# Kernel optimization log

Hardware: AMD Instinct MI355X
Metric: run time of the kernel (lower is better)

The kernel has to match this reference:

```python
import jax, jax.numpy as jnp
import numpy as np

IMG = 800          # image size (square)
STRIDE = 4         # feature-map stride
S = 14             # rcnn_crop_size
C = 256            # crop_channels
N = 512            # number of rpn proposals
NUM_CLASSES = 81   # COCO (incl. background at index 0)
HID = 1024
NMS_TH = 0.5
SCORE_TH = 0.05


def setup_inputs() -> dict:
    key = jax.random.key(0)
    ks = jax.random.split(key, 8)
    features = jax.random.normal(ks[0], (1, C, IMG // STRIDE, IMG // STRIDE), jnp.float32)
    # valid proposal boxes (x0, y0, x1, y1) in image coordinates
    u = jax.random.uniform(ks[1], (N, 4), jnp.float32)
    x0 = u[:, 0] * (IMG - 64.0)
    y0 = u[:, 1] * (IMG - 64.0)
    bw = 16.0 + u[:, 2] * 240.0
    bh = 16.0 + u[:, 3] * 240.0
    proposals = jnp.stack([x0, y0, jnp.minimum(x0 + bw, IMG - 1.0), jnp.minimum(y0 + bh, IMG - 1.0)], axis=1)
    d1 = C * S * S  # 50176
    w1 = jax.random.normal(ks[2], (d1, HID), jnp.float32) * (1.0 / np.sqrt(d1))
    b1 = jnp.zeros((HID,), jnp.float32)
    w2 = jax.random.normal(ks[3], (HID, HID), jnp.float32) * (1.0 / np.sqrt(HID))
    b2 = jnp.zeros((HID,), jnp.float32)
    w_cls = jax.random.normal(ks[4], (HID, NUM_CLASSES), jnp.float32) * (1.0 / np.sqrt(HID))
    b_cls = jnp.zeros((NUM_CLASSES,), jnp.float32)
    w_reg = jax.random.normal(ks[5], (HID, NUM_CLASSES * 4), jnp.float32) * (1.0 / np.sqrt(HID))
    b_reg = jnp.zeros((NUM_CLASSES * 4,), jnp.float32)
    return dict(features=features, proposals=proposals, w1=w1, b1=b1, w2=w2, b2=b2,
                w_cls=w_cls, b_cls=b_cls, w_reg=w_reg, b_reg=b_reg)


def roi_align(feat, boxes):
    """feat: [C,H,W]; boxes: [N,4] image coords -> crops [N,C,S,S] via bilinear sampling (1 sample per bin)."""
    _, H, W = feat.shape
    b = boxes / STRIDE
    t = (jnp.arange(S, dtype=feat.dtype) + 0.5) / S                # [S] bin centers
    xs = b[:, 0:1] + (b[:, 2:3] - b[:, 0:1]) * t                   # [N,S]
    ys = b[:, 1:2] + (b[:, 3:4] - b[:, 1:2]) * t                   # [N,S]
    xx = jnp.broadcast_to(xs[:, None, :], (boxes.shape[0], S, S))  # [N,S,S]
    yy = jnp.broadcast_to(ys[:, :, None], (boxes.shape[0], S, S))
    x0f = jnp.floor(xx); y0f = jnp.floor(yy)
    fx = xx - x0f; fy = yy - y0f
    x0i = jnp.clip(x0f.astype(jnp.int32), 0, W - 1); x1i = jnp.clip(x0i + 1, 0, W - 1)
    y0i = jnp.clip(y0f.astype(jnp.int32), 0, H - 1); y1i = jnp.clip(y0i + 1, 0, H - 1)
    # gathers -> [C,N,S,S]
    v = (((1 - fx) * (1 - fy))[None] * feat[:, y0i, x0i]
         + (fx * (1 - fy))[None] * feat[:, y0i, x1i]
         + ((1 - fx) * fy)[None] * feat[:, y1i, x0i]
         + (fx * fy)[None] * feat[:, y1i, x1i])
    return v.transpose(1, 0, 2, 3)  # [N,C,S,S]


def decode_boxes(rois, d):
    w = rois[:, 2] - rois[:, 0]; h = rois[:, 3] - rois[:, 1]
    cx = rois[:, 0] + 0.5 * w; cy = rois[:, 1] + 0.5 * h
    px = cx + d[:, 0] * w; py = cy + d[:, 1] * h
    pw = w * jnp.exp(jnp.clip(d[:, 2], -4.0, 4.0))
    ph = h * jnp.exp(jnp.clip(d[:, 3], -4.0, 4.0))
    b = jnp.stack([px - 0.5 * pw, py - 0.5 * ph, px + 0.5 * pw, py + 0.5 * ph], axis=1)
    return jnp.clip(b, 0.0, IMG - 1.0)


def iou_matrix(b):
    area = jnp.maximum(b[:, 2] - b[:, 0], 0.0) * jnp.maximum(b[:, 3] - b[:, 1], 0.0)
    ix0 = jnp.maximum(b[:, None, 0], b[None, :, 0])
    iy0 = jnp.maximum(b[:, None, 1], b[None, :, 1])
    ix1 = jnp.minimum(b[:, None, 2], b[None, :, 2])
    iy1 = jnp.minimum(b[:, None, 3], b[None, :, 3])
    inter = jnp.maximum(ix1 - ix0, 0.0) * jnp.maximum(iy1 - iy0, 0.0)
    return inter / (area[:, None] + area[None, :] - inter + 1e-6)


def reference(features, proposals, w1, b1, w2, b2, w_cls, b_cls, w_reg, b_reg):
    # 1) RoIAlign crop
    crops = roi_align(features[0], proposals)              # [N,C,S,S]
    # 2) RCNN head
    x = crops.reshape(N, -1)
    x = jax.nn.relu(x @ w1 + b1)
    x = jax.nn.relu(x @ w2 + b2)
    logits = x @ w_cls + b_cls                             # [N,81]
    deltas = (x @ w_reg + b_reg).reshape(N, NUM_CLASSES, 4)
    # 3) NMS post-processing
    probs = jax.nn.softmax(logits, axis=-1)
    fg = probs[:, 1:]                                      # exclude background
    labels = jnp.argmax(fg, axis=-1) + 1                   # [N]
    scores = jnp.max(fg, axis=-1)                          # [N]
    d = deltas[jnp.arange(N), labels]                      # per-ROI delta of predicted class
    boxes = decode_boxes(proposals, d)
    order = jnp.argsort(-scores)
    bs = boxes[order]; ss = scores[order]; ls = labels[order]
    valid = ss > SCORE_TH
    M = iou_matrix(bs)                                     # [N,N]
    idx = jnp.arange(N)
    def body(i, keep):
        alive = keep[i] & valid[i]
        supp = (M[i] > NMS_TH) & (idx > i) & alive
        return keep & (~supp)
    keep = jax.lax.fori_loop(0, N, body, valid)
    keepf = jax.lax.stop_gradient(keep.astype(bs.dtype))
    final = jnp.concatenate([bs, ss[:, None]], axis=1) * keepf[:, None]   # [N,5]
    return final, ls.astype(jnp.int32), keep
```

## Files before the change

kernel.cpp:

```cpp
#include <hip/hip_runtime.h>
#include <cstdint>

#define F_H 200
#define F_W 200
#define D1  50176
#define NBOX 512
#define NHID 1024

typedef _Float16 f16;
typedef _Float16 half8 __attribute__((ext_vector_type(8)));
typedef _Float16 half4v __attribute__((ext_vector_type(4)));
typedef _Float16 half2v __attribute__((ext_vector_type(2)));
typedef float    f32x4 __attribute__((ext_vector_type(4)));

__device__ __forceinline__ void gload16(const void* g, void* l) {
  __builtin_amdgcn_global_load_lds((const __attribute__((address_space(1))) void*)g,
                                   (__attribute__((address_space(3))) void*)l,
                                   16, 0, 0);
}

__device__ __forceinline__ half2v pkrtz(float a, float b) {
  return __builtin_bit_cast(half2v, __builtin_amdgcn_cvt_pkrtz(a, b));
}

__device__ __forceinline__ void splitf16(float v, f16& h, f16& l) {
  f16 hh = (f16)v;
  float hf = (float)hh;
  if (fabsf(hf) < 6.1035156e-5f) hf = 0.f;
  h = (f16)hh;
  if (fabsf(hf) < 6.1035156e-5f) h = (f16)0.f;
  l = (f16)((v - hf) * 2048.f);
}

__global__ __launch_bounds__(256) void k_roi(const float* __restrict__ feat,
                                             const float* __restrict__ prop,
                                             f16* __restrict__ xhi, f16* __restrict__ xlo) {
  uint32_t idx = blockIdx.x * 256u + threadIdx.x;
  uint32_t n = idx / 25088u;
  uint32_t rem = idx % 25088u;
  uint32_t c = rem / 98u;
  uint32_t r2 = rem % 98u;
  uint32_t i = r2 / 7u;
  uint32_t jp = r2 % 7u;
  float b0 = prop[n * 4 + 0] * 0.25f, b1 = prop[n * 4 + 1] * 0.25f;
  float b2 = prop[n * 4 + 2] * 0.25f, b3 = prop[n * 4 + 3] * 0.25f;
  float ty = ((float)i + 0.5f) * (1.0f / 14.0f);
  float yy = b1 + (b3 - b1) * ty;
  float y0f = floorf(yy);
  float fy = yy - y0f;
  int y0 = (int)y0f; y0 = y0 < 0 ? 0 : (y0 > F_H - 1 ? F_H - 1 : y0);
  int y1 = y0 + 1 > F_H - 1 ? F_H - 1 : y0 + 1;
  const float* fr0 = feat + (size_t)c * (F_H * F_W) + (size_t)y0 * F_W;
  const float* fr1 = feat + (size_t)c * (F_H * F_W) + (size_t)y1 * F_W;
  f16 hs[2], ls[2];
#pragma unroll
  for (int e = 0; e < 2; ++e) {
    uint32_t j = jp * 2u + (uint32_t)e;
    float tx = ((float)j + 0.5f) * (1.0f / 14.0f);
    float xx = b0 + (b2 - b0) * tx;
    float x0f = floorf(xx);
    float fx = xx - x0f;
    int x0 = (int)x0f; x0 = x0 < 0 ? 0 : (x0 > F_W - 1 ? F_W - 1 : x0);
    int x1 = x0 + 1 > F_W - 1 ? F_W - 1 : x0 + 1;
    float v00 = fr0[x0], v01 = fr0[x1], v10 = fr1[x0], v11 = fr1[x1];
    float v = (1.f - fx) * (1.f - fy) * v00 + fx * (1.f - fy) * v01 +
              (1.f - fx) * fy * v10 + fx * fy * v11;
    splitf16(v, hs[e], ls[e]);
  }
  uint32_t base = n * 50176u + c * 196u + i * 14u + jp * 2u;
  half2v hv; hv[0] = hs[0]; hv[1] = hs[1];
  half2v lv; lv[0] = ls[0]; lv[1] = ls[1];
  *(half2v*)(xhi + base) = hv;
  *(half2v*)(xlo + base) = lv;
}

__global__ __launch_bounds__(256) void k_tsplit(const float* __restrict__ W,
                                                f16* __restrict__ hiT, f16* __restrict__ loT,
                                                int Kdim, int Ndim) {
  __shared__ f16 lh[64 * 72];
  __shared__ f16 ll[64 * 72];
  int t = threadIdx.x;
  int k0 = blockIdx.x * 64, n0 = blockIdx.y * 64;
  int r = t >> 2, cq = t & 3;
  const float* src = W + (size_t)(k0 + r) * Ndim + n0 + cq * 16;
  f16 hv[16], lv[16];
#pragma unroll
  for (int e = 0; e < 4; ++e) {
    f32x4 v = *(const f32x4*)(src + e * 4);
#pragma unroll
    for (int x = 0; x < 4; ++x) splitf16(v[x], hv[e * 4 + x], lv[e * 4 + x]);
  }
#pragma unroll
  for (int j = 0; j < 16; ++j) {
    int n_l = cq * 16 + j;
    lh[n_l * 72 + r] = hv[j];
    ll[n_l * 72 + r] = lv[j];
  }
  __syncthreads();
  f16* oh = hiT + (size_t)(n0 + r) * Kdim + k0 + cq * 16;
  f16* ol = loT + (size_t)(n0 + r) * Kdim + k0 + cq * 16;
  *(half8*)(oh)     = *(const half8*)(&lh[r * 72 + cq * 16]);
  *(half8*)(oh + 8) = *(const half8*)(&lh[r * 72 + cq * 16 + 8]);
  *(half8*)(ol)     = *(const half8*)(&ll[r * 72 + cq * 16]);
  *(half8*)(ol + 8) = *(const half8*)(&ll[r * 72 + cq * 16 + 8]);
}

__global__ __launch_bounds__(256) void k_packT(const float* __restrict__ wc_, const float* __restrict__ bc,
                                               const float* __restrict__ wr_, const float* __restrict__ br,
                                               f16* __restrict__ whT_hi, f16* __restrict__ whT_lo,
                                               float* __restrict__ bh) {
  uint32_t idx = blockIdx.x * 256u + threadIdx.x;
  if (idx < 512u * 1024u) {
    uint32_t n = idx >> 10, k = idx & 1023u;
    float v = 0.f;
    if (n < 81u) v = wc_[k * 81u + n];
    else if (n < 405u) v = wr_[k * 324u + (n - 81u)];
    f16 h, l; splitf16(v, h, l);
    whT_hi[idx] = h; whT_lo[idx] = l;
  } else if (idx < 512u * 1024u + 512u) {
    uint32_t n = idx - 512u * 1024u;
    float v = 0.f;
    if (n < 81u) v = bc[n];
    else if (n < 405u) v = br[n - 81u];
    bh[n] = v;
  }
}

__global__ __launch_bounds__(256) void k_pack(const float* __restrict__ wc, const float* __restrict__ bc,
                                              const float* __restrict__ wr, const float* __restrict__ br,
                                              float* __restrict__ wh, float* __restrict__ bh) {
  uint32_t idx = blockIdx.x * 256u + threadIdx.x;
  if (idx < (uint32_t)NHID * 512u) {
    uint32_t k = idx >> 9, n = idx & 511u;
    float v = 0.f;
    if (n < 81u) v = wc[k * 81u + n];
    else if (n < 405u) v = wr[k * 324u + (n - 81u)];
    wh[idx] = v;
  } else if (idx < (uint32_t)NHID * 512u + 512u) {
    uint32_t n = idx - (uint32_t)NHID * 512u;
    float v = 0.f;
    if (n < 81u) v = bc[n];
    else if (n < 405u) v = br[n - 81u];
    bh[n] = v;
  }
}

__global__ __launch_bounds__(512, 2) void k_gemm2(
    const f16* __restrict__ Ahi, const f16* __restrict__ Alo,
    const f16* __restrict__ Bhi, const f16* __restrict__ Blo,
    float* __restrict__ Cp, int K, int N, int Kc, int nMt, int nNt)
{
  __shared__ char sm[131072];
  const int t = threadIdx.x;
  const int lane = t & 63;
  const int wid = t >> 6;
  const int wr = wid >> 2;
  const int wc = wid & 3;
  const int rl = lane & 15;
  const int lq = lane >> 4;

  int bid = blockIdx.x;
  int low = bid & 7, qq = bid >> 3;
  int nt = qq % nNt;
  int chi = qq / nNt;
  int c = chi * 8 + low;
  int ks = c / nMt;
  int mt = c % nMt;
  const int brow = mt * 256;
  const int nbase = nt * 256;
  const int k0 = ks * Kc;
  const int nk = Kc >> 5;

  uint32_t aoffg[2], aldso[2];
#pragma unroll
  for (int i = 0; i < 2; ++i) {
    uint32_t idx = (uint32_t)t + 512u * i;
    uint32_t q2 = idx >> 2, s = idx & 3;
    uint32_t qh = q2 >> 6;
    uint32_t grh = (qh == 1u) ? 2u : (qh == 2u) ? 1u : qh;
    uint32_t gr = grh * 64u + (q2 & 63u);
    aoffg[i] = (uint32_t)(brow + gr) * (uint32_t)K + (s ^ ((q2 >> 1) & 3u)) * 8u;
    aldso[i] = idx * 16u;
  }
  uint32_t boffg[2], bldso[2];
#pragma unroll
  for (int i = 0; i < 2; ++i) {
    uint32_t idx = (uint32_t)t + 512u * i;
    uint32_t rB = idx >> 2, s = idx & 3;
    boffg[i] = (uint32_t)(nbase + rB) * (uint32_t)K + (s ^ ((rB >> 1) & 3u)) * 8u;
    bldso[i] = idx * 16u;
  }

  const uint32_t swzk = (uint32_t)(lq ^ ((rl >> 1) & 3)) * 16u;
  const uint32_t a_off_lane = (uint32_t)(rl * 64) + swzk;
  const uint32_t b_off_lane = (uint32_t)((wc * 16 + rl) * 64) + swzk;

  f32x4 zero4 = {0.f, 0.f, 0.f, 0.f};
  f32x4 acc[8][4];
#pragma unroll
  for (int m = 0; m < 8; ++m)
#pragma unroll
    for (int n = 0; n < 4; ++n) acc[m][n] = zero4;

#define PH0STAGE(LB, KB) do { \
    gload16(Bhi + boffg[0] + (KB), (LB) + 32768 + bldso[0]); \
    gload16(Blo + boffg[0] + (KB), (LB) + 49152 + bldso[0]); \
    gload16(Bhi + boffg[1] + (KB), (LB) + 32768 + bldso[1]); \
    gload16(Blo + boffg[1] + (KB), (LB) + 49152 + bldso[1]); \
    gload16(Ahi + aoffg[0] + (KB), (LB) + aldso[0]); \
    gload16(Alo + aoffg[0] + (KB), (LB) + 16384 + aldso[0]); \
  } while (0)

#define PH1STAGE(LB, KB) do { \
    gload16(Ahi + aoffg[1] + (KB), (LB) + aldso[1]); \
    gload16(Alo + aoffg[1] + (KB), (LB) + 16384 + aldso[1]); \
  } while (0)

#define COMPUTE_PHASE(P) do { \
    half8 bh2[4], bl2[4]; \
    _Pragma("unroll") \
    for (int nf = 0; nf < 4; ++nf) { \
      bh2[nf] = *(const half8*)(lb + 32768 + nf * 4096 + b_off_lane); \
      bl2[nf] = *(const half8*)(lb + 49152 + nf * 4096 + b_off_lane); \
    } \
    __builtin_amdgcn_s_setprio(1); \
    _Pragma("unroll") \
    for (int mm = 0; mm < 4; ++mm) { \
      const char* ab = lb + (P) * 8192 + wr * 4096 + mm * 1024 + a_off_lane; \
      half8 ah = *(const half8*)(ab); \
      half8 al = *(const half8*)(ab + 16384); \
      _Pragma("unroll") \
      for (int nf = 0; nf < 4; ++nf) { \
        acc[(P)*4+mm][nf] = __builtin_amdgcn_mfma_f32_16x16x32_f16(ah, bh2[nf], acc[(P)*4+mm][nf], 0, 0, 0); \
        f32x4 tt = __builtin_amdgcn_mfma_f32_16x16x32_f16(ah, bl2[nf], zero4, 0, 0, 0); \
        tt = __builtin_amdgcn_mfma_f32_16x16x32_f16(al, bh2[nf], tt, 0, 0, 0); \
        acc[(P)*4+mm][nf] += tt * 4.8828125e-4f; \
      } \
    } \
    __builtin_amdgcn_s_setprio(0); \
  } while (0)

  PH0STAGE(sm, (uint32_t)k0);
  PH1STAGE(sm, (uint32_t)k0);

  int cur = 0;
  for (int kt = 0; kt < nk; ++kt) {
    int ktn = (kt + 1 < nk) ? kt + 1 : kt;
    uint32_t kbn = (uint32_t)(k0 + ktn * 32);
    const char* lb = sm + cur * 65536;
    char* lbn = sm + (cur ^ 1) * 65536;

    asm volatile("s_waitcnt vmcnt(2)" ::: "memory");
    __builtin_amdgcn_s_barrier();
    __builtin_amdgcn_sched_barrier(0);
    PH0STAGE(lbn, kbn);
    COMPUTE_PHASE(0);

    asm volatile("s_waitcnt vmcnt(6)" ::: "memory");
    __builtin_amdgcn_s_barrier();
    __builtin_amdgcn_sched_barrier(0);
    PH1STAGE(lbn, kbn);
    COMPUTE_PHASE(1);

    cur ^= 1;
  }

  float* Cs = Cp + (size_t)ks * ((size_t)512 * (uint32_t)N);
#pragma unroll
  for (int m = 0; m < 8; ++m) {
    int rg = brow + wr * 128 + m * 16 + lq * 4;
#pragma unroll
    for (int nf = 0; nf < 4; ++nf) {
      int cg = nbase + nf * 64 + wc * 16 + rl;
#pragma unroll
      for (int rr = 0; rr < 4; ++rr)
        Cs[(size_t)(rg + rr) * (uint32_t)N + cg] = acc[m][nf][rr];
    }
  }
#undef PH0STAGE
#undef PH1STAGE
#undef COMPUTE_PHASE
}

__global__ __launch_bounds__(512, 2) void k_gemm(
    const f16* __restrict__ Ahi, const f16* __restrict__ Alo,
    const float* __restrict__ B, float* __restrict__ Cp,
    int K, int N, int Kc, int nMt, int nNt)
{
  __shared__ char sm[131072];
  const int t = threadIdx.x;
  const int lane = t & 63;
  const int wid = t >> 6;
  const int wr = wid >> 2;
  const int wc = wid & 3;
  const int rl = lane & 15;
  const int lq = lane >> 4;

  int bid = blockIdx.x;
  int low = bid & 7, q = bid >> 3;
  int nt = q % nNt;
  int chi = q / nNt;
  int c = chi * 8 + low;
  int ks = c / nMt;
  int mt = c % nMt;
  const int brow = mt * 256;
  const int nbase = nt * 256;
  const int k0 = ks * Kc;
  const int nk = Kc >> 5;

  uint32_t aoffg[2], aldso[2];
#pragma unroll
  for (int i = 0; i < 2; ++i) {
    uint32_t idx = (uint32_t)t + 512u * i;
    uint32_t r = idx >> 2, s = idx & 3;
    uint32_t sz = s ^ ((r >> 1) & 3);
    aoffg[i] = (uint32_t)(brow + r) * (uint32_t)K + sz * 8u;
    aldso[i] = idx * 16u;
  }
  uint32_t boffg[2][2], bldso[2][2];
#pragma unroll
  for (int h = 0; h < 2; ++h)
#pragma unroll
    for (int i = 0; i < 2; ++i) {
      uint32_t idx = (uint32_t)t + 512u * i;
      uint32_t kr = idx >> 5, sg = idx & 31;
      uint32_t sgs = sg ^ (((kr >> 3) & 3) << 2);
      boffg[h][i] = kr * (uint32_t)N + (uint32_t)(nbase + h * 128) + sgs * 4u;
      bldso[h][i] = 32768u + (uint32_t)h * 16384u + idx * 16u;
    }

  const uint32_t a_off = (uint32_t)(wr * 8192 + rl * 64) + (uint32_t)((lq ^ ((rl >> 1) & 3)) * 16);
  const uint32_t b_lane = (uint32_t)((((wc ^ lq) & 3) * 16 + rl) * 4);

  f32x4 zero4 = {0.f, 0.f, 0.f, 0.f};
  f32x4 acc[8][4];
#pragma unroll
  for (int m = 0; m < 8; ++m)
#pragma unroll
    for (int n = 0; n < 4; ++n) acc[m][n] = zero4;

#define STAGE_A(LB, KB) do { \
    gload16(Ahi + aoffg[0] + (KB), (LB) + aldso[0]); \
    gload16(Alo + aoffg[0] + (KB), (LB) + 16384 + aldso[0]); \
    gload16(Ahi + aoffg[1] + (KB), (LB) + aldso[1]); \
    gload16(Alo + aoffg[1] + (KB), (LB) + 16384 + aldso[1]); \
  } while (0)

#define STAGE_B(LB, KB) do { \
    gload16(B + (size_t)(KB) * (uint32_t)N + boffg[0][0], (LB) + bldso[0][0]); \
    gload16(B + (size_t)(KB) * (uint32_t)N + boffg[0][1], (LB) + bldso[0][1]); \
    gload16(B + (size_t)(KB) * (uint32_t)N + boffg[1][0], (LB) + bldso[1][0]); \
    gload16(B + (size_t)(KB) * (uint32_t)N + boffg[1][1], (LB) + bldso[1][1]); \
  } while (0)

#define COMPUTE_PHASE(P) do { \
    half8 bhv[2], blv[2]; \
    _Pragma("unroll") \
    for (int x = 0; x < 2; ++x) { \
      const int nf = 2 * (P) + x; \
      const char* bb = lb + 32768 + (nf >> 1) * 16384 + (nf & 1) * 256 + b_lane; \
      _Pragma("unroll") \
      for (int jj = 0; jj < 8; jj += 2) { \
        float v0 = *(const float*)(bb + (lq * 8 + jj) * 512); \
        float v1 = *(const float*)(bb + (lq * 8 + jj + 1) * 512); \
        half2v hp = pkrtz(v0, v1); \
        f16 e0 = (fabsf(v0) >= 6.1035156e-5f) ? hp[0] : (f16)0; \
        f16 e1 = (fabsf(v1) >= 6.1035156e-5f) ? hp[1] : (f16)0; \
        half2v lp = pkrtz((v0 - (float)e0) * 2048.f, (v1 - (float)e1) * 2048.f); \
        bhv[x][jj] = e0; bhv[x][jj + 1] = e1; \
        blv[x][jj] = lp[0]; blv[x][jj + 1] = lp[1]; \
      } \
    } \
    __builtin_amdgcn_s_setprio(1); \
    _Pragma("unroll") \
    for (int m = 0; m < 8; ++m) { \
      half8 ah = *(const half8*)(lb + a_off + m * 1024); \
      half8 al = *(const half8*)(lb + 16384 + a_off + m * 1024); \
      _Pragma("unroll") \
      for (int x = 0; x < 2; ++x) { \
        const int nf = 2 * (P) + x; \
        acc[m][nf] = __builtin_amdgcn_mfma_f32_16x16x32_f16(ah, bhv[x], acc[m][nf], 0, 0, 0); \
        f32x4 tt = __builtin_amdgcn_mfma_f32_16x16x32_f16(ah, blv[x], zero4, 0, 0, 0); \
        tt = __builtin_amdgcn_mfma_f32_16x16x32_f16(al, bhv[x], tt, 0, 0, 0); \
        acc[m][nf] += tt * 4.8828125e-4f; \
      } \
    } \
    __builtin_amdgcn_s_setprio(0); \
  } while (0)

  STAGE_A(sm, (uint32_t)k0);
  STAGE_B(sm, (uint32_t)k0);

  int cur = 0;
  for (int kt = 0; kt < nk; ++kt) {
    int ktn = (kt + 1 < nk) ? kt + 1 : kt;
    uint32_t kbn = (uint32_t)(k0 + ktn * 32);
    const char* lb = sm + cur * 65536;
    char* lbn = sm + (cur ^ 1) * 65536;

    asm volatile("s_waitcnt vmcnt(2)" ::: "memory");
    __builtin_amdgcn_s_barrier();
    __builtin_amdgcn_sched_barrier(0);
    STAGE_A(lbn, kbn);
    COMPUTE_PHASE(0);

    asm volatile("s_waitcnt vmcnt(4)" ::: "memory");
    __builtin_amdgcn_s_barrier();
    __builtin_amdgcn_sched_barrier(0);
    STAGE_B(lbn, kbn);
    COMPUTE_PHASE(1);

    cur ^= 1;
  }

  float* Cs = Cp + (size_t)ks * ((size_t)512 * (uint32_t)N);
#pragma unroll
  for (int m = 0; m < 8; ++m) {
    int rg = brow + wr * 128 + m * 16 + lq * 4;
#pragma unroll
    for (int nf = 0; nf < 4; ++nf) {
      int cg = nbase + nf * 64 + wc * 16 + rl;
#pragma unroll
      for (int rr = 0; rr < 4; ++rr)
        Cs[(size_t)(rg + rr) * (uint32_t)N + cg] = acc[m][nf][rr];
    }
  }
#undef STAGE_A
#undef STAGE_B
#undef COMPUTE_PHASE
}

__global__ __launch_bounds__(256) void k_reduce(
    const float* __restrict__ parts, const float* __restrict__ bias,
    int nS, int MN4, int Ncols, int relu,
    float* __restrict__ outf, f16* __restrict__ ohi, f16* __restrict__ olo)
{
  uint32_t idx = blockIdx.x * 256u + threadIdx.x;
  if (idx >= (uint32_t)MN4) return;
  f32x4 s = *(const f32x4*)(bias + ((idx * 4u) % (uint32_t)Ncols));
  const f32x4* p4 = (const f32x4*)parts;
  for (int i = 0; i < nS; ++i) s += p4[(size_t)i * (uint32_t)MN4 + idx];
  if (relu) {
#pragma unroll
    for (int j = 0; j < 4; ++j) s[j] = fmaxf(s[j], 0.f);
  }
  if (outf) *(f32x4*)(outf + (size_t)idx * 4) = s;
  if (ohi) {
    half4v h, l;
#pragma unroll
    for (int j = 0; j < 4; ++j) { f16 hh, ll; splitf16(s[j], hh, ll); h[j] = hh; l[j] = ll; }
    *(half4v*)(ohi + (size_t)idx * 4) = h;
    *(half4v*)(olo + (size_t)idx * 4) = l;
  }
}

__global__ __launch_bounds__(256) void k_post(
    const float* __restrict__ ld, const float* __restrict__ prop,
    float* __restrict__ boxes, float* __restrict__ scores, int* __restrict__ labels)
{
  int n = blockIdx.x * 256 + threadIdx.x;
  if (n >= NBOX) return;
  const float* L = ld + (size_t)n * 512;
  float m = L[0];
  for (int j = 1; j < 81; ++j) m = fmaxf(m, L[j]);
  float sum = 0.f;
  for (int j = 0; j < 81; ++j) sum += expf(L[j] - m);
  float best = -1.f; int bj = 1;
  for (int j = 1; j < 81; ++j) {
    float p = expf(L[j] - m) / sum;
    if (p > best) { best = p; bj = j; }
  }
  float d0 = L[81 + bj * 4 + 0];
  float d1 = L[81 + bj * 4 + 1];
  float d2 = L[81 + bj * 4 + 2];
  float d3 = L[81 + bj * 4 + 3];
  float p0 = prop[n * 4 + 0], p1 = prop[n * 4 + 1], p2 = prop[n * 4 + 2], p3 = prop[n * 4 + 3];
  float w = p2 - p0, h = p3 - p1;
  float cx = p0 + 0.5f * w, cy = p1 + 0.5f * h;
  float px = cx + d0 * w, py = cy + d1 * h;
  float pw = w * expf(fminf(fmaxf(d2, -4.f), 4.f));
  float ph = h * expf(fminf(fmaxf(d3, -4.f), 4.f));
  float bx0 = px - 0.5f * pw, by0 = py - 0.5f * ph;
  float bx1 = px + 0.5f * pw, by1 = py + 0.5f * ph;
  boxes[n * 4 + 0] = fminf(fmaxf(bx0, 0.f), 799.f);
  boxes[n * 4 + 1] = fminf(fmaxf(by0, 0.f), 799.f);
  boxes[n * 4 + 2] = fminf(fmaxf(bx1, 0.f), 799.f);
  boxes[n * 4 + 3] = fminf(fmaxf(by1, 0.f), 799.f);
  scores[n] = best;
  labels[n] = bj;
}

__global__ __launch_bounds__(512) void k_sort(
    const float* __restrict__ scores, const float* __restrict__ boxes, const int* __restrict__ labels,
    float* __restrict__ bs, float* __restrict__ ss, int* __restrict__ ls)
{
  __shared__ unsigned long long keys[512];
  int t = threadIdx.x;
  unsigned sb = __float_as_uint(scores[t]);
  keys[t] = ((unsigned long long)(0xFFFFFFFFu - sb) << 32) | (unsigned)t;
  __syncthreads();
  for (int k = 2; k <= 512; k <<= 1) {
    for (int j = k >> 1; j > 0; j >>= 1) {
      int p = t ^ j;
      if (p > t) {
        unsigned long long a = keys[t], b = keys[p];
        bool asc = ((t & k) == 0);
        if (asc ? (a > b) : (a < b)) { keys[t] = b; keys[p] = a; }
      }
      __syncthreads();
    }
  }
  unsigned o = (unsigned)(keys[t] & 0xFFFFFFFFu);
  ss[t] = scores[o];
  ls[t] = labels[o];
  bs[t * 4 + 0] = boxes[o * 4 + 0];
  bs[t * 4 + 1] = boxes[o * 4 + 1];
  bs[t * 4 + 2] = boxes[o * 4 + 2];
  bs[t * 4 + 3] = boxes[o * 4 + 3];
}

__global__ __launch_bounds__(64) void k_mask(const float* __restrict__ bs,
                                             unsigned long long* __restrict__ mask) {
  int i = blockIdx.x;
  int lane = threadIdx.x;
  float ax0 = bs[i * 4], ay0 = bs[i * 4 + 1], ax1 = bs[i * 4 + 2], ay1 = bs[i * 4 + 3];
  float aarea = fmaxf(ax1 - ax0, 0.f) * fmaxf(ay1 - ay0, 0.f);
  for (int w = 0; w < 8; ++w) {
    int j = w * 64 + lane;
    float bx0 = bs[j * 4], by0 = bs[j * 4 + 1], bx1 = bs[j * 4 + 2], by1 = bs[j * 4 + 3];
    float barea = fmaxf(bx1 - bx0, 0.f) * fmaxf(by1 - by0, 0.f);
    float ix0 = fmaxf(ax0, bx0), iy0 = fmaxf(ay0, by0);
    float ix1 = fminf(ax1, bx1), iy1 = fminf(ay1, by1);
    float inter = fmaxf(ix1 - ix0, 0.f) * fmaxf(iy1 - iy0, 0.f);
    float iou = inter / (aarea + barea - inter + 1e-6f);
    bool cond = (iou > 0.5f) && (j > i);
    unsigned long long b = __ballot(cond);
    if (lane == 0) mask[i * 8 + w] = b;
  }
}

__global__ __launch_bounds__(64) void k_nms(const unsigned long long* __restrict__ mask,
                                            const float* __restrict__ ss,
                                            const float* __restrict__ bs,
                                            const int* __restrict__ ls,
                                            float* __restrict__ out) {
  int lane = threadIdx.x;
  unsigned long long bal[8];
  for (int w = 0; w < 8; ++w) bal[w] = __ballot(ss[w * 64 + lane] > 0.05f);
  unsigned long long keep = (lane < 8) ? bal[lane] : 0ULL;
  for (int i = 0; i < 512; ++i) {
    unsigned long long kw = __shfl(keep, i >> 6);
    if ((kw >> (i & 63)) & 1ULL) {
      unsigned long long mi = (lane < 8) ? mask[i * 8 + lane] : 0ULL;
      keep &= ~mi;
    }
  }
  __shared__ unsigned long long kws[8];
  if (lane < 8) kws[lane] = keep;
  __syncthreads();
  for (int it = 0; it < 56; ++it) {
    int idx = lane + it * 64;
    float val;
    if (idx < 2560) {
      int i = idx / 5, c2 = idx % 5;
      bool kb = (kws[i >> 6] >> (i & 63)) & 1ULL;
      val = kb ? (c2 < 4 ? bs[i * 4 + c2] : ss[i]) : 0.f;
    } else if (idx < 3072) {
      int i = idx - 2560;
      val = (float)ls[i];
    } else {
      int i = idx - 3072;
      val = ((kws[i >> 6] >> (i & 63)) & 1ULL) ? 1.f : 0.f;
    }
    out[idx] = val;
  }
}

static constexpr size_t SZ_X    = (size_t)NBOX * D1 * 2;
static constexpr size_t OFF_XHI = 0;
static constexpr size_t OFF_XLO = OFF_XHI + SZ_X;
static constexpr size_t OFF_PART = OFF_XLO + SZ_X;
static constexpr size_t SZ_PART = (size_t)32 * 512 * 1024 * 4;
static constexpr size_t SZ_H    = (size_t)512 * 1024 * 2;
static constexpr size_t OFF_H1HI = OFF_PART + SZ_PART;
static constexpr size_t OFF_H1LO = OFF_H1HI + SZ_H;
static constexpr size_t OFF_H2HI = OFF_H1LO + SZ_H;
static constexpr size_t OFF_H2LO = OFF_H2HI + SZ_H;
static constexpr size_t OFF_WH   = OFF_H2LO + SZ_H;
static constexpr size_t OFF_BH   = OFF_WH + (size_t)1024 * 512 * 4;
static constexpr size_t OFF_LD   = OFF_BH + 4096;
static constexpr size_t OFF_BOX  = OFF_LD + (size_t)512 * 512 * 4;
static constexpr size_t OFF_SC   = OFF_BOX + 512 * 4 * 4;
static constexpr size_t OFF_LB   = OFF_SC + 4096;
static constexpr size_t OFF_BS   = OFF_LB + 4096;
static constexpr size_t OFF_SS   = OFF_BS + 512 * 4 * 4;
static constexpr size_t OFF_LS   = OFF_SS + 4096;
static constexpr size_t OFF_MASK = OFF_LS + 4096;
static constexpr size_t OFF_END  = OFF_MASK + (size_t)512 * 8 * 8;

static constexpr size_t SZ_W1P   = (size_t)1024 * D1 * 2;
static constexpr size_t NP_XHI   = 0;
static constexpr size_t NP_XLO   = NP_XHI + SZ_X;
static constexpr size_t NP_W1HIT = NP_XLO + SZ_X;
static constexpr size_t NP_W1LOT = NP_W1HIT + SZ_W1P;
static constexpr size_t NP_PART  = NP_W1LOT + SZ_W1P;
static constexpr size_t NP_W2HIT = NP_PART + SZ_PART;
static constexpr size_t NP_W2LOT = NP_W2HIT + (size_t)1024 * 1024 * 2;
static constexpr size_t NP_WHHIT = NP_W2LOT + (size_t)1024 * 1024 * 2;
static constexpr size_t NP_WHLOT = NP_WHHIT + (size_t)512 * 1024 * 2;
static constexpr size_t NP_BH    = NP_WHLOT + (size_t)512 * 1024 * 2;
static constexpr size_t NP_H1HI  = NP_BH + 4096;
static constexpr size_t NP_H1LO  = NP_H1HI + SZ_H;
static constexpr size_t NP_H2HI  = NP_H1LO + SZ_H;
static constexpr size_t NP_H2LO  = NP_H2HI + SZ_H;
static constexpr size_t NP_LD    = NP_H2LO + SZ_H;
static constexpr size_t NP_BOX   = NP_LD + (size_t)512 * 512 * 4;
static constexpr size_t NP_SC    = NP_BOX + 512 * 4 * 4;
static constexpr size_t NP_LB    = NP_SC + 4096;
static constexpr size_t NP_BS    = NP_LB + 4096;
static constexpr size_t NP_SS    = NP_BS + 512 * 4 * 4;
static constexpr size_t NP_LS    = NP_SS + 4096;
static constexpr size_t NP_MASK  = NP_LS + 4096;
static constexpr size_t NP_END   = NP_MASK + (size_t)512 * 8 * 8;

extern "C" void kernel_launch(void* const* d_in, const int* in_sizes, int n_in,
                              void* d_out, int out_size, void* d_ws, size_t ws_size,
                              hipStream_t stream)
{
  (void)in_sizes; (void)n_in;
  const float* feat = (const float*)d_in[0];
  const float* prop = (const float*)d_in[1];
  const float* w1   = (const float*)d_in[2];
  const float* b1   = (const float*)d_in[3];
  const float* w2   = (const float*)d_in[4];
  const float* b2   = (const float*)d_in[5];
  const float* wcls = (const float*)d_in[6];
  const float* bcls = (const float*)d_in[7];
  const float* wreg = (const float*)d_in[8];
  const float* breg = (const float*)d_in[9];
  float* out = (float*)d_out;
  char* W = (char*)d_ws;

  if (ws_size >= NP_END) {
    f16*   xhi   = (f16*)(W + NP_XHI);
    f16*   xlo   = (f16*)(W + NP_XLO);
    f16*   w1hiT = (f16*)(W + NP_W1HIT);
    f16*   w1loT = (f16*)(W + NP_W1LOT);
    float* parts = (float*)(W + NP_PART);
    f16*   w2hiT = (f16*)(W + NP_W2HIT);
    f16*   w2loT = (f16*)(W + NP_W2LOT);
    f16*   whHiT = (f16*)(W + NP_WHHIT);
    f16*   whLoT = (f16*)(W + NP_WHLOT);
    float* bhead = (float*)(W + NP_BH);
    f16*   h1hi  = (f16*)(W + NP_H1HI);
    f16*   h1lo  = (f16*)(W + NP_H1LO);
    f16*   h2hi  = (f16*)(W + NP_H2HI);
    f16*   h2lo  = (f16*)(W + NP_H2LO);
    float* ldbuf = (float*)(W + NP_LD);
    float* boxes = (float*)(W + NP_BOX);
    float* scores= (float*)(W + NP_SC);
    int*   labels= (int*)(W + NP_LB);
    float* bsrt  = (float*)(W + NP_BS);
    float* ssrt  = (float*)(W + NP_SS);
    int*   lsrt  = (int*)(W + NP_LS);
    unsigned long long* maskb = (unsigned long long*)(W + NP_MASK);

    k_tsplit<<<dim3(D1 / 64, 1024 / 64), 256, 0, stream>>>(w1, w1hiT, w1loT, D1, 1024);
    k_roi<<<50176, 256, 0, stream>>>(feat, prop, xhi, xlo);
    k_tsplit<<<dim3(1024 / 64, 1024 / 64), 256, 0, stream>>>(w2, w2hiT, w2loT, 1024, 1024);
    k_packT<<<2050, 256, 0, stream>>>(wcls, bcls, wreg, breg, whHiT, whLoT, bhead);

    k_gemm2<<<256, 512, 0, stream>>>(xhi, xlo, w1hiT, w1loT, parts, D1, 1024, 1568, 2, 4);
    k_reduce<<<512, 256, 0, stream>>>(parts, b1, 32, 131072, 1024, 1, nullptr, h1hi, h1lo);

    k_gemm2<<<256, 512, 0, stream>>>(h1hi, h1lo, w2hiT, w2loT, parts, 1024, 1024, 32, 2, 4);
    k_reduce<<<512, 256, 0, stream>>>(parts, b2, 32, 131072, 1024, 1, nullptr, h2hi, h2lo);

    k_gemm2<<<128, 512, 0, stream>>>(h2hi, h2lo, whHiT, whLoT, parts, 1024, 512, 32, 2, 2);
    k_reduce<<<256, 256, 0, stream>>>(parts, bhead, 32, 65536, 512, 0, ldbuf, nullptr, nullptr);

    k_post<<<2, 256, 0, stream>>>(ldbuf, prop, boxes, scores, labels);
    k_sort<<<1, 512, 0, stream>>>(scores, boxes, labels, bsrt, ssrt, lsrt);
    k_mask<<<512, 64, 0, stream>>>(bsrt, maskb);
    k_nms<<<1, 64, 0, stream>>>(maskb, ssrt, bsrt, lsrt, out);
    return;
  }

  if (ws_size < OFF_END) {
    (void)hipMemsetAsync(out, 0x7f, (size_t)out_size * 4, stream);
    return;
  }

  f16*   xhi   = (f16*)(W + OFF_XHI);
  f16*   xlo   = (f16*)(W + OFF_XLO);
  float* parts = (float*)(W + OFF_PART);
  f16*   h1hi  = (f16*)(W + OFF_H1HI);
  f16*   h1lo  = (f16*)(W + OFF_H1LO);
  f16*   h2hi  = (f16*)(W + OFF_H2HI);
  f16*   h2lo  = (f16*)(W + OFF_H2LO);
  float* whead = (float*)(W + OFF_WH);
  float* bhead = (float*)(W + OFF_BH);
  float* ldbuf = (float*)(W + OFF_LD);
  float* boxes = (float*)(W + OFF_BOX);
  float* scores= (float*)(W + OFF_SC);
  int*   labels= (int*)(W + OFF_LB);
  float* bsrt  = (float*)(W + OFF_BS);
  float* ssrt  = (float*)(W + OFF_SS);
  int*   lsrt  = (int*)(W + OFF_LS);
  unsigned long long* maskb = (unsigned long long*)(W + OFF_MASK);

  k_pack<<<2050, 256, 0, stream>>>(wcls, bcls, wreg, breg, whead, bhead);
  k_roi<<<50176, 256, 0, stream>>>(feat, prop, xhi, xlo);

  k_gemm<<<256, 512, 0, stream>>>(xhi, xlo, w1, parts, D1, 1024, 1568, 2, 4);
  k_reduce<<<512, 256, 0, stream>>>(parts, b1, 32, 131072, 1024, 1, nullptr, h1hi, h1lo);

  k_gemm<<<64, 512, 0, stream>>>(h1hi, h1lo, w2, parts, 1024, 1024, 128, 2, 4);
  k_reduce<<<512, 256, 0, stream>>>(parts, b2, 8, 131072, 1024, 1, nullptr, h2hi, h2lo);

  k_gemm<<<64, 512, 0, stream>>>(h2hi, h2lo, whead, parts, 1024, 512, 64, 2, 2);
  k_reduce<<<256, 256, 0, stream>>>(parts, bhead, 16, 65536, 512, 0, ldbuf, nullptr, nullptr);

  k_post<<<2, 256, 0, stream>>>(ldbuf, prop, boxes, scores, labels);
  k_sort<<<1, 512, 0, stream>>>(scores, boxes, labels, bsrt, ssrt, lsrt);
  k_mask<<<512, 64, 0, stream>>>(bsrt, maskb);
  k_nms<<<1, 64, 0, stream>>>(maskb, ssrt, bsrt, lsrt, out);
}
```

Baseline: 477.9 us.

## Split fp32 W1 into hi/lo fp16 inside GEMM instead of pre-pass

Drops the separate k_tsplit pre-pass over the 50176x1024 W1 matrix and the workspace it needed. A new k_gemm3 loads raw fp32 W1 through registers, splits it into hi/lo fp16 once per element, and writes transposed swizzled tiles into LDS. The old in-loop split ran inside every compute phase. The first layer now reads W1 only once per GEMM, at the cost of register-staged loads and plain __syncthreads double buffering instead of async global-to-LDS loads. The fallback path is merged into a single path that uses the pre-split W2 and head weights.

```diff
diff --git a/kernel.cpp b/kernel.cpp
--- a/kernel.cpp
+++ b/kernel.cpp
@@ -119,25 +119,6 @@
     whT_hi[idx] = h; whT_lo[idx] = l;
   } else if (idx < 512u * 1024u + 512u) {
     uint32_t n = idx - 512u * 1024u;
-    float v = 0.f;
-    if (n < 81u) v = bc[n];
-    else if (n < 405u) v = br[n - 81u];
-    bh[n] = v;
-  }
-}
-
-__global__ __launch_bounds__(256) void k_pack(const float* __restrict__ wc, const float* __restrict__ bc,
-                                              const float* __restrict__ wr, const float* __restrict__ br,
-                                              float* __restrict__ wh, float* __restrict__ bh) {
-  uint32_t idx = blockIdx.x * 256u + threadIdx.x;
-  if (idx < (uint32_t)NHID * 512u) {
-    uint32_t k = idx >> 9, n = idx & 511u;
-    float v = 0.f;
-    if (n < 81u) v = wc[k * 81u + n];
-    else if (n < 405u) v = wr[k * 324u + (n - 81u)];
-    wh[idx] = v;
-  } else if (idx < (uint32_t)NHID * 512u + 512u) {
-    uint32_t n = idx - (uint32_t)NHID * 512u;
     float v = 0.f;
     if (n < 81u) v = bc[n];
     else if (n < 405u) v = br[n - 81u];
@@ -279,10 +260,9 @@
   }
 #undef PH0STAGE
 #undef PH1STAGE
-#undef COMPUTE_PHASE
-}
-
-__global__ __launch_bounds__(512, 2) void k_gemm(
+}
+
+__global__ __launch_bounds__(512, 2) void k_gemm3(
     const f16* __restrict__ Ahi, const f16* __restrict__ Alo,
     const float* __restrict__ B, float* __restrict__ Cp,
     int K, int N, int Kc, int nMt, int nNt)
@@ -297,9 +277,9 @@
   const int lq = lane >> 4;
 
   int bid = blockIdx.x;
-  int low = bid & 7, q = bid >> 3;
-  int nt = q % nNt;
-  int chi = q / nNt;
+  int low = bid & 7, qq = bid >> 3;
+  int nt = qq % nNt;
+  int chi = qq / nNt;
   int c = chi * 8 + low;
   int ks = c / nMt;
   int mt = c % nMt;
@@ -312,25 +292,24 @@
 #pragma unroll
   for (int i = 0; i < 2; ++i) {
     uint32_t idx = (uint32_t)t + 512u * i;
-    uint32_t r = idx >> 2, s = idx & 3;
-    uint32_t sz = s ^ ((r >> 1) & 3);
-    aoffg[i] = (uint32_t)(brow + r) * (uint32_t)K + sz * 8u;
+    uint32_t q2 = idx >> 2, s = idx & 3;
+    uint32_t qh = q2 >> 6;
+    uint32_t grh = (qh == 1u) ? 2u : (qh == 2u) ? 1u : qh;
+    uint32_t gr = grh * 64u + (q2 & 63u);
+    aoffg[i] = (uint32_t)(brow + gr) * (uint32_t)K + (s ^ ((q2 >> 1) & 3u)) * 8u;
     aldso[i] = idx * 16u;
   }
-  uint32_t boffg[2][2], bldso[2][2];
-#pragma unroll
-  for (int h = 0; h < 2; ++h)
-#pragma unroll
-    for (int i = 0; i < 2; ++i) {
-      uint32_t idx = (uint32_t)t + 512u * i;
-      uint32_t kr = idx >> 5, sg = idx & 31;
-      uint32_t sgs = sg ^ (((kr >> 3) & 3) << 2);
-      boffg[h][i] = kr * (uint32_t)N + (uint32_t)(nbase + h * 128) + sgs * 4u;
-      bldso[h][i] = 32768u + (uint32_t)h * 16384u + idx * 16u;
-    }
-
-  const uint32_t a_off = (uint32_t)(wr * 8192 + rl * 64) + (uint32_t)((lq ^ ((rl >> 1) & 3)) * 16);
-  const uint32_t b_lane = (uint32_t)((((wc ^ lq) & 3) * 16 + rl) * 4);
+
+  const uint32_t nrow = (uint32_t)t & 255u;
+  const uint32_t kh = (uint32_t)t >> 8;
+  const float* bsrc0 = B + (size_t)((uint32_t)k0 + kh * 16u) * (uint32_t)N + (uint32_t)nbase + nrow;
+  const uint32_t bswz = (nrow >> 1) & 3u;
+  const uint32_t wb0 = nrow * 64u + (((kh * 2u)      ^ bswz) << 4);
+  const uint32_t wb1 = nrow * 64u + (((kh * 2u + 1u) ^ bswz) << 4);
+
+  const uint32_t swzk = (uint32_t)(lq ^ ((rl >> 1) & 3)) * 16u;
+  const uint32_t a_off_lane = (uint32_t)(rl * 64) + swzk;
+  const uint32_t b_off_lane = (uint32_t)((wc * 16 + rl) * 64) + swzk;
 
   f32x4 zero4 = {0.f, 0.f, 0.f, 0.f};
   f32x4 acc[8][4];
@@ -339,77 +318,56 @@
 #pragma unroll
     for (int n = 0; n < 4; ++n) acc[m][n] = zero4;
 
-#define STAGE_A(LB, KB) do { \
+  float breg[16];
+
+#define LOADB(KT) do { \
+    const float* bp = bsrc0 + (size_t)((uint32_t)(KT) * 32u) * (uint32_t)N; \
+    _Pragma("unroll") \
+    for (int j = 0; j < 16; ++j) breg[j] = bp[(size_t)j * (uint32_t)N]; \
+  } while (0)
+
+#define WRITEB(LB) do { \
+    half8 h0, l0, h1, l1; \
+    _Pragma("unroll") \
+    for (int j = 0; j < 16; j += 2) { \
+      float v0 = breg[j], v1 = breg[j + 1]; \
+      half2v hp = pkrtz(v0, v1); \
+      f16 e0 = (fabsf(v0) >= 6.1035156e-5f) ? hp[0] : (f16)0; \
+      f16 e1 = (fabsf(v1) >= 6.1035156e-5f) ? hp[1] : (f16)0; \
+      half2v lp = pkrtz((v0 - (float)e0) * 2048.f, (v1 - (float)e1) * 2048.f); \
+      if (j < 8) { h0[j] = e0; h0[j + 1] = e1; l0[j] = lp[0]; l0[j + 1] = lp[1]; } \
+      else { h1[j - 8] = e0; h1[j - 7] = e1; l1[j - 8] = lp[0]; l1[j - 7] = lp[1]; } \
+    } \
+    *(half8*)((LB) + 32768 + wb0) = h0; \
+    *(half8*)((LB) + 49152 + wb0) = l0; \
+    *(half8*)((LB) + 32768 + wb1) = h1; \
+    *(half8*)((LB) + 49152 + wb1) = l1; \
+  } while (0)
+
+#define STAGE_A4(LB, KB) do { \
     gload16(Ahi + aoffg[0] + (KB), (LB) + aldso[0]); \
     gload16(Alo + aoffg[0] + (KB), (LB) + 16384 + aldso[0]); \
     gload16(Ahi + aoffg[1] + (KB), (LB) + aldso[1]); \
     gload16(Alo + aoffg[1] + (KB), (LB) + 16384 + aldso[1]); \
   } while (0)
 
-#define STAGE_B(LB, KB) do { \
-    gload16(B + (size_t)(KB) * (uint32_t)N + boffg[0][0], (LB) + bldso[0][0]); \
-    gload16(B + (size_t)(KB) * (uint32_t)N + boffg[0][1], (LB) + bldso[0][1]); \
-    gload16(B + (size_t)(KB) * (uint32_t)N + boffg[1][0], (LB) + bldso[1][0]); \
-    gload16(B + (size_t)(KB) * (uint32_t)N + boffg[1][1], (LB) + bldso[1][1]); \
-  } while (0)
-
-#define COMPUTE_PHASE(P) do { \
-    half8 bhv[2], blv[2]; \
-    _Pragma("unroll") \
-    for (int x = 0; x < 2; ++x) { \
-      const int nf = 2 * (P) + x; \
-      const char* bb = lb + 32768 + (nf >> 1) * 16384 + (nf & 1) * 256 + b_lane; \
-      _Pragma("unroll") \
-      for (int jj = 0; jj < 8; jj += 2) { \
-        float v0 = *(const float*)(bb + (lq * 8 + jj) * 512); \
-        float v1 = *(const float*)(bb + (lq * 8 + jj + 1) * 512); \
-        half2v hp = pkrtz(v0, v1); \
-        f16 e0 = (fabsf(v0) >= 6.1035156e-5f) ? hp[0] : (f16)0; \
-        f16 e1 = (fabsf(v1) >= 6.1035156e-5f) ? hp[1] : (f16)0; \
-        half2v lp = pkrtz((v0 - (float)e0) * 2048.f, (v1 - (float)e1) * 2048.f); \
-        bhv[x][jj] = e0; bhv[x][jj + 1] = e1; \
-        blv[x][jj] = lp[0]; blv[x][jj + 1] = lp[1]; \
-      } \
-    } \
-    __builtin_amdgcn_s_setprio(1); \
-    _Pragma("unroll") \
-    for (int m = 0; m < 8; ++m) { \
-      half8 ah = *(const half8*)(lb + a_off + m * 1024); \
-      half8 al = *(const half8*)(lb + 16384 + a_off + m * 1024); \
-      _Pragma("unroll") \
-      for (int x = 0; x < 2; ++x) { \
-        const int nf = 2 * (P) + x; \
-        acc[m][nf] = __builtin_amdgcn_mfma_f32_16x16x32_f16(ah, bhv[x], acc[m][nf], 0, 0, 0); \
-        f32x4 tt = __builtin_amdgcn_mfma_f32_16x16x32_f16(ah, blv[x], zero4, 0, 0, 0); \
-        tt = __builtin_amdgcn_mfma_f32_16x16x32_f16(al, bhv[x], tt, 0, 0, 0); \
-        acc[m][nf] += tt * 4.8828125e-4f; \
-      } \
-    } \
-    __builtin_amdgcn_s_setprio(0); \
-  } while (0)
-
-  STAGE_A(sm, (uint32_t)k0);
-  STAGE_B(sm, (uint32_t)k0);
+  LOADB(0);
+  STAGE_A4(sm, (uint32_t)k0);
+  WRITEB(sm);
+  __syncthreads();
 
   int cur = 0;
   for (int kt = 0; kt < nk; ++kt) {
     int ktn = (kt + 1 < nk) ? kt + 1 : kt;
-    uint32_t kbn = (uint32_t)(k0 + ktn * 32);
     const char* lb = sm + cur * 65536;
     char* lbn = sm + (cur ^ 1) * 65536;
 
-    asm volatile("s_waitcnt vmcnt(2)" ::: "memory");
-    __builtin_amdgcn_s_barrier();
-    __builtin_amdgcn_sched_barrier(0);
-    STAGE_A(lbn, kbn);
+    LOADB(ktn);
+    STAGE_A4(lbn, (uint32_t)(k0 + ktn * 32));
     COMPUTE_PHASE(0);
-
-    asm volatile("s_waitcnt vmcnt(4)" ::: "memory");
-    __builtin_amdgcn_s_barrier();
-    __builtin_amdgcn_sched_barrier(0);
-    STAGE_B(lbn, kbn);
+    WRITEB(lbn);
     COMPUTE_PHASE(1);
-
+    __syncthreads();
     cur ^= 1;
   }
 
@@ -425,8 +383,9 @@
         Cs[(size_t)(rg + rr) * (uint32_t)N + cg] = acc[m][nf][rr];
     }
   }
-#undef STAGE_A
-#undef STAGE_B
+#undef LOADB
+#undef WRITEB
+#undef STAGE_A4
 #undef COMPUTE_PHASE
 }
 
@@ -577,33 +536,11 @@
 }
 
 static constexpr size_t SZ_X    = (size_t)NBOX * D1 * 2;
-static constexpr size_t OFF_XHI = 0;
-static constexpr size_t OFF_XLO = OFF_XHI + SZ_X;
-static constexpr size_t OFF_PART = OFF_XLO + SZ_X;
 static constexpr size_t SZ_PART = (size_t)32 * 512 * 1024 * 4;
 static constexpr size_t SZ_H    = (size_t)512 * 1024 * 2;
-static constexpr size_t OFF_H1HI = OFF_PART + SZ_PART;
-static constexpr size_t OFF_H1LO = OFF_H1HI + SZ_H;
-static constexpr size_t OFF_H2HI = OFF_H1LO + SZ_H;
-static constexpr size_t OFF_H2LO = OFF_H2HI + SZ_H;
-static constexpr size_t OFF_WH   = OFF_H2LO + SZ_H;
-static constexpr size_t OFF_BH   = OFF_WH + (size_t)1024 * 512 * 4;
-static constexpr size_t OFF_LD   = OFF_BH + 4096;
-static constexpr size_t OFF_BOX  = OFF_LD + (size_t)512 * 512 * 4;
-static constexpr size_t OFF_SC   = OFF_BOX + 512 * 4 * 4;
-static constexpr size_t OFF_LB   = OFF_SC + 4096;
-static constexpr size_t OFF_BS   = OFF_LB + 4096;
-static constexpr size_t OFF_SS   = OFF_BS + 512 * 4 * 4;
-static constexpr size_t OFF_LS   = OFF_SS + 4096;
-static constexpr size_t OFF_MASK = OFF_LS + 4096;
-static constexpr size_t OFF_END  = OFF_MASK + (size_t)512 * 8 * 8;
-
-static constexpr size_t SZ_W1P   = (size_t)1024 * D1 * 2;
 static constexpr size_t NP_XHI   = 0;
 static constexpr size_t NP_XLO   = NP_XHI + SZ_X;
-static constexpr size_t NP_W1HIT = NP_XLO + SZ_X;
-static constexpr size_t NP_W1LOT = NP_W1HIT + SZ_W1P;
-static constexpr size_t NP_PART  = NP_W1LOT + SZ_W1P;
+static constexpr size_t NP_PART  = NP_XLO + SZ_X;
 static constexpr size_t NP_W2HIT = NP_PART + SZ_PART;
 static constexpr size_t NP_W2LOT = NP_W2HIT + (size_t)1024 * 1024 * 2;
 static constexpr size_t NP_WHHIT = NP_W2LOT + (size_t)1024 * 1024 * 2;
@@ -641,85 +578,44 @@
   float* out = (float*)d_out;
   char* W = (char*)d_ws;
 
-  if (ws_size >= NP_END) {
-    f16*   xhi   = (f16*)(W + NP_XHI);
-    f16*   xlo   = (f16*)(W + NP_XLO);
-    f16*   w1hiT = (f16*)(W + NP_W1HIT);
-    f16*   w1loT = (f16*)(W + NP_W1LOT);
-    float* parts = (float*)(W + NP_PART);
-    f16*   w2hiT = (f16*)(W + NP_W2HIT);
-    f16*   w2loT = (f16*)(W + NP_W2LOT);
-    f16*   whHiT = (f16*)(W + NP_WHHIT);
-    f16*   whLoT = (f16*)(W + NP_WHLOT);
-    float* bhead = (float*)(W + NP_BH);
-    f16*   h1hi  = (f16*)(W + NP_H1HI);
-    f16*   h1lo  = (f16*)(W + NP_H1LO);
-    f16*   h2hi  = (f16*)(W + NP_H2HI);
-    f16*   h2lo  = (f16*)(W + NP_H2LO);
-    float* ldbuf = (float*)(W + NP_LD);
-    float* boxes = (float*)(W + NP_BOX);
-    float* scores= (float*)(W + NP_SC);
-    int*   labels= (int*)(W + NP_LB);
-    float* bsrt  = (float*)(W + NP_BS);
-    float* ssrt  = (float*)(W + NP_SS);
-    int*   lsrt  = (int*)(W + NP_LS);
-    unsigned long long* maskb = (unsigned long long*)(W + NP_MASK);
-
-    k_tsplit<<<dim3(D1 / 64, 1024 / 64), 256, 0, stream>>>(w1, w1hiT, w1loT, D1, 1024);
-    k_roi<<<50176, 256, 0, stream>>>(feat, prop, xhi, xlo);
-    k_tsplit<<<dim3(1024 / 64, 1024 / 64), 256, 0, stream>>>(w2, w2hiT, w2loT, 1024, 1024);
-    k_packT<<<2050, 256, 0, stream>>>(wcls, bcls, wreg, breg, whHiT, whLoT, bhead);
-
-    k_gemm2<<<256, 512, 0, stream>>>(xhi, xlo, w1hiT, w1loT, parts, D1, 1024, 1568, 2, 4);
-    k_reduce<<<512, 256, 0, stream>>>(parts, b1, 32, 131072, 1024, 1, nullptr, h1hi, h1lo);
-
-    k_gemm2<<<256, 512, 0, stream>>>(h1hi, h1lo, w2hiT, w2loT, parts, 1024, 1024, 32, 2, 4);
-    k_reduce<<<512, 256, 0, stream>>>(parts, b2, 32, 131072, 1024, 1, nullptr, h2hi, h2lo);
-
-    k_gemm2<<<128, 512, 0, stream>>>(h2hi, h2lo, whHiT, whLoT, parts, 1024, 512, 32, 2, 2);
-    k_reduce<<<256, 256, 0, stream>>>(parts, bhead, 32, 65536, 512, 0, ldbuf, nullptr, nullptr);
-
-    k_post<<<2, 256, 0, stream>>>(ldbuf, prop, boxes, scores, labels);
-    k_sort<<<1, 512, 0, stream>>>(scores, boxes, labels, bsrt, ssrt, lsrt);
-    k_mask<<<512, 64, 0, stream>>>(bsrt, maskb);
-    k_nms<<<1, 64, 0, stream>>>(maskb, ssrt, bsrt, lsrt, out);
-    return;
-  }
-
-  if (ws_size < OFF_END) {
+  if (ws_size < NP_END) {
     (void)hipMemsetAsync(out, 0x7f, (size_t)out_size * 4, stream);
     return;
   }
 
-  f16*   xhi   = (f16*)(W + OFF_XHI);
-  f16*   xlo   = (f16*)(W + OFF_XLO);
-  float* parts = (float*)(W + OFF_PART);
-  f16*   h1hi  = (f16*)(W + OFF_H1HI);
-  f16*   h1lo  = (f16*)(W + OFF_H1LO);
-  f16*   h2hi  = (f16*)(W + OFF_H2HI);
-  f16*   h2lo  = (f16*)(W + OFF_H2LO);
-  float* whead = (float*)(W + OFF_WH);
-  float* bhead = (float*)(W + OFF_BH);
-  float* ldbuf = (float*)(W + OFF_LD);
-  float* boxes = (float*)(W + OFF_BOX);
-  float* scores= (float*)(W + OFF_SC);
-  int*   labels= (int*)(W + OFF_LB);
-  float* bsrt  = (float*)(W + OFF_BS);
-  float* ssrt  = (float*)(W + OFF_SS);
-  int*   lsrt  = (int*)(W + OFF_LS);
-  unsigned long long* maskb = (unsigned long long*)(W + OFF_MASK);
-
-  k_pack<<<2050, 256, 0, stream>>>(wcls, bcls, wreg, breg, whead, bhead);
+  f16*   xhi   = (f16*)(W + NP_XHI);
+  f16*   xlo   = (f16*)(W + NP_XLO);
+  float* parts = (float*)(W + NP_PART);
+  f16*   w2hiT = (f16*)(W + NP_W2HIT);
+  f16*   w2loT = (f16*)(W + NP_W2LOT);
+  f16*   whHiT = (f16*)(W + NP_WHHIT);
+  f16*   whLoT = (f16*)(W + NP_WHLOT);
+  float* bhead = (float*)(W + NP_BH);
+  f16*   h1hi  = (f16*)(W + NP_H1HI);
+  f16*   h1lo  = (f16*)(W + NP_H1LO);
+  f16*   h2hi  = (f16*)(W + NP_H2HI);
+  f16*   h2lo  = (f16*)(W + NP_H2LO);
+  float* ldbuf = (float*)(W + NP_LD);
+  float* boxes = (float*)(W + NP_BOX);
+  float* scores= (float*)(W + NP_SC);
+  int*   labels= (int*)(W + NP_LB);
+  float* bsrt  = (float*)(W + NP_BS);
+  float* ssrt  = (float*)(W + NP_SS);
+  int*   lsrt  = (int*)(W + NP_LS);
+  unsigned long long* maskb = (unsigned long long*)(W + NP_MASK);
+
   k_roi<<<50176, 256, 0, stream>>>(feat, prop, xhi, xlo);
-
-  k_gemm<<<256, 512, 0, stream>>>(xhi, xlo, w1, parts, D1, 1024, 1568, 2, 4);
+  k_tsplit<<<dim3(1024 / 64, 1024 / 64), 256, 0, stream>>>(w2, w2hiT, w2loT, 1024, 1024);
+  k_packT<<<2050, 256, 0, stream>>>(wcls, bcls, wreg, breg, whHiT, whLoT, bhead);
+
+  k_gemm3<<<256, 512, 0, stream>>>(xhi, xlo, w1, parts, D1, 1024, 1568, 2, 4);
   k_reduce<<<512, 256, 0, stream>>>(parts, b1, 32, 131072, 1024, 1, nullptr, h1hi, h1lo);
 
-  k_gemm<<<64, 512, 0, stream>>>(h1hi, h1lo, w2, parts, 1024, 1024, 128, 2, 4);
-  k_reduce<<<512, 256, 0, stream>>>(parts, b2, 8, 131072, 1024, 1, nullptr, h2hi, h2lo);
-
-  k_gemm<<<64, 512, 0, stream>>>(h2hi, h2lo, whead, parts, 1024, 512, 64, 2, 2);
-  k_reduce<<<256, 256, 0, stream>>>(parts, bhead, 16, 65536, 512, 0, ldbuf, nullptr, nullptr);
+  k_gemm2<<<256, 512, 0, stream>>>(h1hi, h1lo, w2hiT, w2loT, parts, 1024, 1024, 32, 2, 4);
+  k_reduce<<<512, 256, 0, stream>>>(parts, b2, 32, 131072, 1024, 1, nullptr, h2hi, h2lo);
+
+  k_gemm2<<<128, 512, 0, stream>>>(h2hi, h2lo, whHiT, whLoT, parts, 1024, 512, 32, 2, 2);
+  k_reduce<<<256, 256, 0, stream>>>(parts, bhead, 32, 65536, 512, 0, ldbuf, nullptr, nullptr);
 
   k_post<<<2, 256, 0, stream>>>(ldbuf, prop, boxes, scores, labels);
   k_sort<<<1, 512, 0, stream>>>(scores, boxes, labels, bsrt, ssrt, lsrt);
```

Measured after the change: 434.6 us. -9.1%, faster.
